# Kernel optimization log

Hardware: AMD Instinct MI355X
Metric: run time of the kernel (lower is better)

Reference implementation:

```python
import jax, jax.numpy as jnp
import numpy as np

LATENT_DIM = 128
NUM_QUANTIZERS = 8
CODEBOOK_SIZE = 1024


def setup_inputs() -> dict:
    key = jax.random.key(0)
    k1, k2 = jax.random.split(key)
    z = jax.random.normal(k1, (8, LATENT_DIM, 4096), dtype=jnp.float32)
    scale = 1.0 / np.sqrt(LATENT_DIM)
    codebooks = jax.random.uniform(
        k2, (NUM_QUANTIZERS, CODEBOOK_SIZE, LATENT_DIM),
        minval=-scale, maxval=scale, dtype=jnp.float32)
    return {"z": z, "codebooks": codebooks}


def _nearest_indices(x_flat, codebook):
    # x_flat: [N, D], codebook: [K, D] -> [N] argmin of squared L2 distance
    d = (jnp.sum(x_flat * x_flat, axis=1, keepdims=True)
         - 2.0 * x_flat @ codebook.T
         + jnp.sum(codebook * codebook, axis=1)[None, :])
    return jnp.argmin(d, axis=1)


def reference(z, codebooks):
    # z: [B, D, S] -> z_bsd: [B, S, D]
    z_bsd = jnp.transpose(z, (0, 2, 1))
    B, S, D = z_bsd.shape
    Q, K, _ = codebooks.shape

    residual = z_bsd
    quantized = jnp.zeros_like(z_bsd)
    idx_list = []
    for q in range(Q):  # small fixed loop over quantizer stages
        cb = codebooks[q]
        idx = _nearest_indices(residual.reshape(-1, D), cb).reshape(B, S)
        selected = cb[idx]                       # [B, S, D] gather
        quantized = quantized + selected
        residual = residual - jax.lax.stop_gradient(selected)
        idx_list.append(idx)
    indices = jnp.stack(idx_list, axis=-1)        # [B, S, Q]

    commitment_loss = jnp.mean(
        (z_bsd - jax.lax.stop_gradient(quantized)) ** 2)
    quantized_st = z_bsd + jax.lax.stop_gradient(quantized - z_bsd)

    def _perplexity(ix):  # ix: [B, S] codes for one quantizer
        counts = jnp.zeros((K,), jnp.float32).at[ix.reshape(-1)].add(1.0)
        probs = counts / jnp.maximum(counts.sum(), 1.0)
        entropy = -jnp.sum(probs * jnp.log(probs + 1e-10))
        return jnp.exp(entropy)

    perplexity = jnp.mean(jax.vmap(_perplexity, in_axes=2)(indices))

    return (jnp.transpose(quantized_st, (0, 2, 1)),  # [B, D, S]
            indices, commitment_loss, perplexity)
```

## Files before the change

kernel.cpp:

```cpp
#include <hip/hip_runtime.h>
#include <math.h>
#include <stdint.h>

#define D       128
#define KCODES  1024
#define NQ      8
#define BATCH   8
#define SLEN    4096
#define NPTS    (BATCH*SLEN)
#define TM      64

typedef __attribute__((address_space(1))) const void GV;
typedef __attribute__((address_space(3))) void LV;
__device__ __forceinline__ void gload16(const void* g, void* l) {
    __builtin_amdgcn_global_load_lds((GV*)g, (LV*)l, 16, 0, 0);
}

__global__ void k_zero(int* hist, double* csum) {
    int t = blockIdx.x * blockDim.x + threadIdx.x;
    if (t < NQ * KCODES) hist[t] = 0;
    if (t == 0) *csum = 0.0;
}

__global__ void k_c2(const float* __restrict__ cbs, float* __restrict__ c2f) {
    int i = blockIdx.x * blockDim.x + threadIdx.x;
    const float* row = cbs + (size_t)i * D;
    float r8[8];
    #pragma unroll
    for (int j = 0; j < 8; ++j) r8[j] = __fmul_rn(row[j], row[j]);
    for (int d = 8; d < 128; d += 8)
        #pragma unroll
        for (int j = 0; j < 8; ++j)
            r8[j] = __fadd_rn(r8[j], __fmul_rn(row[d + j], row[d + j]));
    float s01 = __fadd_rn(r8[0], r8[1]);
    float s23 = __fadd_rn(r8[2], r8[3]);
    float s45 = __fadd_rn(r8[4], r8[5]);
    float s67 = __fadd_rn(r8[6], r8[7]);
    c2f[i] = __fadd_rn(__fadd_rn(s01, s23), __fadd_rn(s45, s67));
}

__global__ __launch_bounds__(256) void k_init(const float* __restrict__ z,
                                              float* __restrict__ resid,
                                              float* __restrict__ quant) {
    __shared__ float xt[64][129];
    int b = blockIdx.x >> 6, st = blockIdx.x & 63;
    int s0 = st * 64;
    for (int it = 0; it < 32; ++it) {
        int flat = it * 256 + threadIdx.x;
        int d = flat >> 6, sl = flat & 63;
        xt[sl][d] = z[((size_t)(b * D + d)) * SLEN + s0 + sl];
    }
    __syncthreads();
    for (int it = 0; it < 8; ++it) {
        int flat = it * 256 + threadIdx.x;
        int sl = flat >> 5, dq = (flat & 31) * 4;
        size_t o = (size_t)(b * SLEN + s0 + sl) * D + dq;
        float4 r;
        r.x = xt[sl][dq]; r.y = xt[sl][dq + 1];
        r.z = xt[sl][dq + 2]; r.w = xt[sl][dq + 3];
        *(float4*)(resid + o) = r;
        float4 zz; zz.x = zz.y = zz.z = zz.w = 0.0f;
        *(float4*)(quant + o) = zz;
    }
}

__global__ __launch_bounds__(256) void k_argmin(const float* __restrict__ cb,
                                                const float* __restrict__ c2,
                                                const float* __restrict__ resid,
                                                int* __restrict__ idx_out) {
    __shared__ __align__(16) float xs[TM][132];
    __shared__ float xxs[TM];
    __shared__ __align__(16) float cs[4][2][1024];
    __shared__ float redS[4][TM];
    __shared__ int   redI[4][TM];

    int tid = threadIdx.x;
    int pbase = blockIdx.x * TM;
    int l = tid & 63, w = tid >> 6;
    int pl = l & 7, cl = l >> 3;

    const char*  cwb = (const char*)cb + ((size_t)w << 17);
    const float* c2w = c2 + (w << 8);

    int gsrc_lane = ((l >> 2) << 9) + ((((l & 3) ^ ((l >> 3) & 3))) << 4);
    int rtau = (cl >> 1) & 3;
    char* csw = (char*)&cs[w][0][0];

    {
        const char* src = cwb + gsrc_lane;
        #pragma unroll
        for (int g = 0; g < 4; ++g)
            gload16(src + (g << 13), csw + (g << 10));
    }

    #pragma unroll
    for (int it = 0; it < 8; ++it) {
        int e = (it * 256 + tid) * 4;
        int p = e >> 7, d = e & 127;
        *(float4*)&xs[p][d] = *(const float4*)(resid + (size_t)(pbase + p) * D + d);
    }
    __syncthreads();

    if (tid < TM) {
        float r8[8];
        #pragma unroll
        for (int j = 0; j < 8; ++j) r8[j] = __fmul_rn(xs[tid][j], xs[tid][j]);
        for (int i = 8; i < 128; i += 8)
            #pragma unroll
            for (int j = 0; j < 8; ++j)
                r8[j] = __fadd_rn(r8[j], __fmul_rn(xs[tid][i + j], xs[tid][i + j]));
        float s01 = __fadd_rn(r8[0], r8[1]);
        float s23 = __fadd_rn(r8[2], r8[3]);
        float s45 = __fadd_rn(r8[4], r8[5]);
        float s67 = __fadd_rn(r8[6], r8[7]);
        xxs[tid] = __fadd_rn(__fadd_rn(s01, s23), __fadd_rn(s45, s67));
    }
    __syncthreads();

    float xxr[8];
    #pragma unroll
    for (int i = 0; i < 8; ++i) xxr[i] = xxs[pl + 8 * i];

    float acc[8][8];
    #pragma unroll
    for (int i = 0; i < 8; ++i)
        #pragma unroll
        for (int j = 0; j < 8; ++j) acc[i][j] = 0.0f;
    float best[8]; int bidx[8];
    #pragma unroll
    for (int i = 0; i < 8; ++i) { best[i] = 3.4e38f; bidx[i] = 0; }

    float cc8[8];
    #pragma unroll 1
    for (int t = 0; t < 32; ++t) {
        int cblk = t >> 3, s = t & 7, buf = t & 1;
        if (s == 0) {
            #pragma unroll
            for (int j = 0; j < 8; ++j)
                cc8[j] = c2w[(cblk << 6) + cl + (j << 3)];
        }
        if (t < 31) {
            int t2 = t + 1;
            const char* src = cwb + gsrc_lane + ((t2 >> 3) << 15) + ((t2 & 7) << 6);
            char* dst = csw + ((t2 & 1) << 12);
            #pragma unroll
            for (int g = 0; g < 4; ++g)
                gload16(src + (g << 13), dst + (g << 10));
            __builtin_amdgcn_sched_barrier(0);
            asm volatile("s_waitcnt vmcnt(4)" ::: "memory");
        } else {
            asm volatile("s_waitcnt vmcnt(0)" ::: "memory");
        }
        const char* cbuf = csw + (buf << 12) + (cl << 6);
        const char* xrow = (const char*)&xs[0][0] + pl * 528 + (s << 6);
        #pragma unroll
        for (int d4 = 0; d4 < 4; ++d4) {
            float4 xf[8], cf[8];
            #pragma unroll
            for (int i = 0; i < 8; ++i)
                xf[i] = *(const float4*)(xrow + i * 4224 + (d4 << 4));
            #pragma unroll
            for (int j = 0; j < 8; ++j)
                cf[j] = *(const float4*)(cbuf + ((d4 ^ rtau) << 4) + (j << 9));
            #pragma unroll
            for (int j = 0; j < 8; ++j)
                #pragma unroll
                for (int i = 0; i < 8; ++i) {
                    acc[i][j] = __fmaf_rn(xf[i].x, cf[j].x, acc[i][j]);
                    acc[i][j] = __fmaf_rn(xf[i].y, cf[j].y, acc[i][j]);
                    acc[i][j] = __fmaf_rn(xf[i].z, cf[j].z, acc[i][j]);
                    acc[i][j] = __fmaf_rn(xf[i].w, cf[j].w, acc[i][j]);
                }
        }
        if (s == 7) {
            #pragma unroll
            for (int j = 0; j < 8; ++j) {
                float cc = cc8[j];
                int k = (w << 8) + (cblk << 6) + cl + (j << 3);
                #pragma unroll
                for (int i = 0; i < 8; ++i) {
                    float t1  = __fadd_rn(xxr[i],
                                          __fmul_rn(-2.0f, acc[i][j]));
                    float dsc = __fadd_rn(t1, cc);
                    if (dsc < best[i]) { best[i] = dsc; bidx[i] = k; }
                    acc[i][j] = 0.0f;
                }
            }
        }
    }

    #pragma unroll
    for (int i = 0; i < 8; ++i) {
        float b = best[i]; int bi = bidx[i];
        #pragma unroll
        for (int off = 8; off < 64; off <<= 1) {
            float b2 = __shfl_xor(b, off, 64);
            int  bi2 = __shfl_xor(bi, off, 64);
            if (b2 < b || (b2 == b && bi2 < bi)) { b = b2; bi = bi2; }
        }
        if (cl == 0) { redS[w][pl + 8 * i] = b; redI[w][pl + 8 * i] = bi; }
    }
    __syncthreads();
    if (tid < TM) {
        float b = redS[0][tid]; int bi = redI[0][tid];
        #pragma unroll
        for (int ww = 1; ww < 4; ++ww) {
            float b2 = redS[ww][tid]; int bi2 = redI[ww][tid];
            if (b2 < b || (b2 == b && bi2 < bi)) { b = b2; bi = bi2; }
        }
        idx_out[pbase + tid] = bi;
    }
}

__global__ void k_update(const float* __restrict__ cb, const int* __restrict__ idx,
                         float* __restrict__ resid, float* __restrict__ quant) {
    int gid = blockIdx.x * blockDim.x + threadIdx.x;
    int n = gid >> 5, d4 = (gid & 31) * 4;
    int k = idx[n];
    float4 c = *(const float4*)(cb + (size_t)k * D + d4);
    size_t o = (size_t)n * D + d4;
    float4 r = *(const float4*)(resid + o);
    float4 q = *(const float4*)(quant + o);
    r.x = __fsub_rn(r.x, c.x); r.y = __fsub_rn(r.y, c.y);
    r.z = __fsub_rn(r.z, c.z); r.w = __fsub_rn(r.w, c.w);
    q.x = __fadd_rn(q.x, c.x); q.y = __fadd_rn(q.y, c.y);
    q.z = __fadd_rn(q.z, c.z); q.w = __fadd_rn(q.w, c.w);
    *(float4*)(resid + o) = r;
    *(float4*)(quant + o) = q;
}

__global__ __launch_bounds__(256) void k_out0(const float* __restrict__ z,
                                              const float* __restrict__ quant,
                                              float* __restrict__ out0,
                                              double* __restrict__ csum) {
    __shared__ float xt[64][129];
    __shared__ double wsum[4];
    int b = blockIdx.x >> 6, st = blockIdx.x & 63;
    int s0 = st * 64;
    for (int it = 0; it < 8; ++it) {
        int flat = it * 256 + threadIdx.x;
        int sl = flat >> 5, dq = (flat & 31) * 4;
        float4 q = *(const float4*)(quant + (size_t)(b * SLEN + s0 + sl) * D + dq);
        xt[sl][dq] = q.x; xt[sl][dq + 1] = q.y;
        xt[sl][dq + 2] = q.z; xt[sl][dq + 3] = q.w;
    }
    __syncthreads();
    double v = 0.0;
    for (int it = 0; it < 32; ++it) {
        int flat = it * 256 + threadIdx.x;
        int d = flat >> 6, sl = flat & 63;
        size_t o = ((size_t)(b * D + d)) * SLEN + s0 + sl;
        float zz = z[o], qq = xt[sl][d];
        out0[o] = __fadd_rn(zz, __fsub_rn(qq, zz));
        float e = __fsub_rn(zz, qq);
        v += (double)e * (double)e;
    }
    for (int off = 32; off > 0; off >>= 1) v += __shfl_down(v, off, 64);
    int lane = threadIdx.x & 63, wv = threadIdx.x >> 6;
    if (lane == 0) wsum[wv] = v;
    __syncthreads();
    if (threadIdx.x == 0) {
        double tsum = wsum[0] + wsum[1] + wsum[2] + wsum[3];
        atomicAdd(csum, tsum);
    }
}

__global__ void k_outidx(const int* __restrict__ idx, float* __restrict__ out1) {
    int o = blockIdx.x * blockDim.x + threadIdx.x;
    int q = o & 7, n = o >> 3;
    out1[o] = (float)idx[q * NPTS + n];
}

__global__ void k_hist(const int* __restrict__ idx, int* __restrict__ hist) {
    int o = blockIdx.x * blockDim.x + threadIdx.x;
    int q = o >> 15;
    atomicAdd(&hist[q * KCODES + idx[o]], 1);
}

__global__ __launch_bounds__(256) void k_final(const int* __restrict__ hist,
                                               const double* __restrict__ csum,
                                               float* __restrict__ outs) {
    __shared__ double sh[256];
    double perp = 0.0;
    for (int q = 0; q < NQ; ++q) {
        double h = 0.0;
        for (int k = threadIdx.x; k < KCODES; k += 256) {
            double p = (double)hist[q * KCODES + k] / (double)NPTS;
            h -= p * log(p + 1e-10);
        }
        sh[threadIdx.x] = h; __syncthreads();
        for (int off = 128; off > 0; off >>= 1) {
            if (threadIdx.x < off) sh[threadIdx.x] += sh[threadIdx.x + off];
            __syncthreads();
        }
        if (threadIdx.x == 0) perp += exp(sh[0]);
        __syncthreads();
    }
    if (threadIdx.x == 0) {
        outs[0] = (float)(*csum / (double)((size_t)NPTS * D));
        outs[1] = (float)(perp / (double)NQ);
    }
}

extern "C" void kernel_launch(void* const* d_in, const int* in_sizes, int n_in,
                              void* d_out, int out_size, void* d_ws, size_t ws_size,
                              hipStream_t stream) {
    const float* z  = (const float*)d_in[0];
    const float* cb = (const float*)d_in[1];
    float* out0 = (float*)d_out;
    float* out1 = out0 + 4194304;
    float* outs = out1 + 262144;

    char* w = (char*)d_ws;
    float* resid  = (float*)w;
    float* quant  = (float*)(w + 16777216);
    int*   idx    = (int*)(w + 33554432);
    int*   hist   = (int*)(w + 34603008);
    double* csum  = (double*)(w + 34635776);
    float* c2f    = (float*)(w + 34635840);

    k_zero<<<32, 256, 0, stream>>>(hist, csum);
    k_c2<<<32, 256, 0, stream>>>(cb, c2f);
    k_init<<<512, 256, 0, stream>>>(z, resid, quant);

    for (int q = 0; q < NQ; ++q) {
        const float* cbq = cb + (size_t)q * KCODES * D;
        k_argmin<<<NPTS / TM, 256, 0, stream>>>(cbq, c2f + q * KCODES, resid,
                                                idx + q * NPTS);
        k_update<<<NPTS * 32 / 256, 256, 0, stream>>>(cbq, idx + q * NPTS,
                                                      resid, quant);
    }

    k_out0<<<512, 256, 0, stream>>>(z, quant, out0, csum);
    k_outidx<<<NPTS * NQ / 256, 256, 0, stream>>>(idx, out1);
    k_hist<<<NPTS * NQ / 256, 256, 0, stream>>>(idx, hist);
    k_final<<<1, 256, 0, stream>>>(hist, csum, outs);
}
```

Before: 1.181 ms.

## Enlarge per-thread codebook tile to 16 codes with 8-dim chunks

Each thread now accumulates an 8x16 register tile (16 codewords per wave lane) instead of 8x8, processing 128 codes per block over 16 dim-chunks of 8 floats. The codebook LDS staging changes to a [128][8] layout without XOR swizzle, and codebook squared norms are preloaded into shared memory once instead of reloaded per block. This raises FMA-to-LDS-load ratio for x operands but doubles accumulator registers, risking lower occupancy or spills and possible LDS bank conflicts without the swizzle.

```diff
diff --git a/kernel.cpp b/kernel.cpp
--- a/kernel.cpp
+++ b/kernel.cpp
@@ -70,7 +70,8 @@
                                                 int* __restrict__ idx_out) {
     __shared__ __align__(16) float xs[TM][132];
     __shared__ float xxs[TM];
-    __shared__ __align__(16) float cs[4][2][1024];
+    __shared__ __align__(16) float cs[4][2][128][8];
+    __shared__ __align__(16) float ccl[4][256];
     __shared__ float redS[4][TM];
     __shared__ int   redI[4][TM];
 
@@ -79,18 +80,21 @@
     int l = tid & 63, w = tid >> 6;
     int pl = l & 7, cl = l >> 3;
 
-    const char*  cwb = (const char*)cb + ((size_t)w << 17);
-    const float* c2w = c2 + (w << 8);
-
-    int gsrc_lane = ((l >> 2) << 9) + ((((l & 3) ^ ((l >> 3) & 3))) << 4);
-    int rtau = (cl >> 1) & 3;
-    char* csw = (char*)&cs[w][0][0];
+    const char* cwb = (const char*)cb + ((size_t)w << 17);
+    int gsrc_lane = ((l >> 1) << 9) + ((l & 1) << 4);
+    char* csw = (char*)&cs[w][0][0][0];
+    const char* xsb = (const char*)&xs[0][0];
 
     {
         const char* src = cwb + gsrc_lane;
-        #pragma unroll
-        for (int g = 0; g < 4; ++g)
-            gload16(src + (g << 13), csw + (g << 10));
+        gload16(src,             csw);
+        gload16(src + (1 << 14), csw + 1024);
+        gload16(src + (2 << 14), csw + 2048);
+        gload16(src + (3 << 14), csw + 3072);
+    }
+    {
+        float4 cv = *(const float4*)(c2 + (w << 8) + l * 4);
+        *(float4*)&ccl[w][l * 4] = cv;
     }
 
     #pragma unroll
@@ -121,66 +125,65 @@
     #pragma unroll
     for (int i = 0; i < 8; ++i) xxr[i] = xxs[pl + 8 * i];
 
-    float acc[8][8];
+    float acc[8][16];
     #pragma unroll
     for (int i = 0; i < 8; ++i)
         #pragma unroll
-        for (int j = 0; j < 8; ++j) acc[i][j] = 0.0f;
+        for (int j = 0; j < 16; ++j) acc[i][j] = 0.0f;
     float best[8]; int bidx[8];
     #pragma unroll
     for (int i = 0; i < 8; ++i) { best[i] = 3.4e38f; bidx[i] = 0; }
 
-    float cc8[8];
     #pragma unroll 1
     for (int t = 0; t < 32; ++t) {
-        int cblk = t >> 3, s = t & 7, buf = t & 1;
-        if (s == 0) {
-            #pragma unroll
-            for (int j = 0; j < 8; ++j)
-                cc8[j] = c2w[(cblk << 6) + cl + (j << 3)];
-        }
+        int c = t >> 4, s = t & 15, buf = t & 1;
         if (t < 31) {
             int t2 = t + 1;
-            const char* src = cwb + gsrc_lane + ((t2 >> 3) << 15) + ((t2 & 7) << 6);
+            const char* src = cwb + gsrc_lane + ((t2 >> 4) << 16) + ((t2 & 15) << 5);
             char* dst = csw + ((t2 & 1) << 12);
-            #pragma unroll
-            for (int g = 0; g < 4; ++g)
-                gload16(src + (g << 13), dst + (g << 10));
-            __builtin_amdgcn_sched_barrier(0);
+            gload16(src,             dst);
+            gload16(src + (1 << 14), dst + 1024);
+            gload16(src + (2 << 14), dst + 2048);
+            gload16(src + (3 << 14), dst + 3072);
             asm volatile("s_waitcnt vmcnt(4)" ::: "memory");
         } else {
             asm volatile("s_waitcnt vmcnt(0)" ::: "memory");
         }
-        const char* cbuf = csw + (buf << 12) + (cl << 6);
-        const char* xrow = (const char*)&xs[0][0] + pl * 528 + (s << 6);
-        #pragma unroll
-        for (int d4 = 0; d4 < 4; ++d4) {
-            float4 xf[8], cf[8];
+        const char* cbuf = csw + (buf << 12) + (cl << 5);
+        const char* xrow = xsb + pl * 528 + (s << 5);
+        #pragma unroll
+        for (int d4 = 0; d4 < 2; ++d4) {
+            float4 xf[8];
             #pragma unroll
             for (int i = 0; i < 8; ++i)
                 xf[i] = *(const float4*)(xrow + i * 4224 + (d4 << 4));
             #pragma unroll
-            for (int j = 0; j < 8; ++j)
-                cf[j] = *(const float4*)(cbuf + ((d4 ^ rtau) << 4) + (j << 9));
+            for (int jb = 0; jb < 4; ++jb) {
+                float4 cf[4];
+                #pragma unroll
+                for (int j = 0; j < 4; ++j)
+                    cf[j] = *(const float4*)(cbuf + ((jb * 4 + j) << 8) + (d4 << 4));
+                #pragma unroll
+                for (int j = 0; j < 4; ++j) {
+                    int jj = jb * 4 + j;
+                    #pragma unroll
+                    for (int i = 0; i < 8; ++i) {
+                        acc[i][jj] = __fmaf_rn(xf[i].x, cf[j].x, acc[i][jj]);
+                        acc[i][jj] = __fmaf_rn(xf[i].y, cf[j].y, acc[i][jj]);
+                        acc[i][jj] = __fmaf_rn(xf[i].z, cf[j].z, acc[i][jj]);
+                        acc[i][jj] = __fmaf_rn(xf[i].w, cf[j].w, acc[i][jj]);
+                    }
+                }
+            }
+        }
+        if (s == 15) {
             #pragma unroll
-            for (int j = 0; j < 8; ++j)
+            for (int j = 0; j < 16; ++j) {
+                float cc = ccl[w][(c << 7) + cl + (j << 3)];
+                int k = (w << 8) + (c << 7) + cl + (j << 3);
                 #pragma unroll
                 for (int i = 0; i < 8; ++i) {
-                    acc[i][j] = __fmaf_rn(xf[i].x, cf[j].x, acc[i][j]);
-                    acc[i][j] = __fmaf_rn(xf[i].y, cf[j].y, acc[i][j]);
-                    acc[i][j] = __fmaf_rn(xf[i].z, cf[j].z, acc[i][j]);
-                    acc[i][j] = __fmaf_rn(xf[i].w, cf[j].w, acc[i][j]);
-                }
-        }
-        if (s == 7) {
-            #pragma unroll
-            for (int j = 0; j < 8; ++j) {
-                float cc = cc8[j];
-                int k = (w << 8) + (cblk << 6) + cl + (j << 3);
-                #pragma unroll
-                for (int i = 0; i < 8; ++i) {
-                    float t1  = __fadd_rn(xxr[i],
-                                          __fmul_rn(-2.0f, acc[i][j]));
+                    float t1  = __fadd_rn(xxr[i], __fmul_rn(-2.0f, acc[i][j]));
                     float dsc = __fadd_rn(t1, cc);
                     if (dsc < best[i]) { best[i] = dsc; bidx[i] = k; }
                     acc[i][j] = 0.0f;
```

After: 1.177 ms. No clear change (-0.3%).
